# Performance work log

Measured on AMD Instinct MI355X. Metric: run time of the kernel, lower is better.

The kernel has to match this reference:

```python
import jax, jax.numpy as jnp
import numpy as np

N_INPUTS, N_NEURONS, N_OUTPUTS = 64, 128, 32
T = 1048576


def setup_inputs() -> dict:
    key = jax.random.key(0)
    ks = jax.random.split(key, 7)
    s = 1.0 / np.sqrt(N_NEURONS)  # PyTorch RNNCell init: U(-1/sqrt(hidden), 1/sqrt(hidden))
    x = jax.random.normal(ks[0], (T, N_INPUTS), dtype=jnp.float32)
    W_ih = jax.random.uniform(ks[1], (N_NEURONS, N_INPUTS), jnp.float32, -s, s)
    W_hh = jax.random.uniform(ks[2], (N_NEURONS, N_NEURONS), jnp.float32, -s, s)
    b_ih = jax.random.uniform(ks[3], (N_NEURONS,), jnp.float32, -s, s)
    b_hh = jax.random.uniform(ks[4], (N_NEURONS,), jnp.float32, -s, s)
    W_out = jax.random.uniform(ks[5], (N_NEURONS, N_OUTPUTS), jnp.float32, -0.01, 0.01)
    b_out = jax.random.uniform(ks[6], (N_OUTPUTS,), jnp.float32, -0.01, 0.01)
    h0 = jnp.zeros((N_NEURONS,), dtype=jnp.float32)  # self.hidden_state, never updated
    return {"external_input_tensor": x, "W_ih": W_ih, "W_hh": W_hh,
            "b_ih": b_ih, "b_hh": b_hh, "W_out": W_out, "b_out": b_out, "h0": h0}


def reference(external_input_tensor, W_ih, W_hh, b_ih, b_hh, W_out, b_out, h0):
    # Original torch loop never updates self.hidden_state, so every step uses h0:
    # h_t = relu(x_t @ W_ih^T + b_ih + h0 @ W_hh^T + b_hh); out_t = h_t @ W_out + b_out
    # This is fully parallel over T, so vectorize the whole thing.
    hidden_drive = h0 @ W_hh.T + b_ih + b_hh  # [N_NEURONS]
    h = jax.nn.relu(external_input_tensor @ W_ih.T + hidden_drive)  # [T, N_NEURONS]
    return h @ W_out + b_out  # [T, N_OUTPUTS]
```

## Files before the change

kernel.cpp:

```cpp
#include <hip/hip_runtime.h>
#include <hip/hip_bf16.h>


typedef __attribute__((ext_vector_type(8))) short short8v;
typedef __attribute__((ext_vector_type(4))) short short4v;
typedef __attribute__((ext_vector_type(4))) float f32x4;

static __device__ __forceinline__ short f2bs(float f) {
    union { __hip_bfloat16 b; short s; } u;
    u.b = __float2bfloat16(f);
    return u.s;
}

static __device__ __forceinline__ short8v pack8(f32x4 a, f32x4 b) {
    short8v r;
    r[0] = f2bs(a[0]); r[1] = f2bs(a[1]); r[2] = f2bs(a[2]); r[3] = f2bs(a[3]);
    r[4] = f2bs(b[0]); r[5] = f2bs(b[1]); r[6] = f2bs(b[2]); r[7] = f2bs(b[3]);
    return r;
}

__global__ void hd_kernel(const float* __restrict__ Whh, const float* __restrict__ bih,
                          const float* __restrict__ bhh, const float* __restrict__ h0,
                          float* __restrict__ hd) {
    int n = threadIdx.x;
    if (n < 128) {
        float s = bih[n] + bhh[n];
        for (int k = 0; k < 128; ++k) s += Whh[n * 128 + k] * h0[k];
        hd[n] = s;
    }
}

#define HSTRIDE 136

__global__ __launch_bounds__(256, 2)
void rnn_fused(const float* __restrict__ x, const float* __restrict__ Wih,
               const float* __restrict__ Wout, const float* __restrict__ bout,
               const float* __restrict__ hd, float* __restrict__ out, int T) {
    const int lane = threadIdx.x & 63;
    const int wave = threadIdx.x >> 6;
    const int c    = lane & 15;
    const int q    = lane >> 4;
    const int nwaves = gridDim.x * 4;
    const int gw     = blockIdx.x * 4 + wave;
    const int NT     = T >> 4;

    __shared__ __align__(16) short hbuf[4 * 16 * HSTRIDE];
    short* hrow = &hbuf[wave * (16 * HSTRIDE)];

    short8v a_w[8][2];
#pragma unroll
    for (int mt = 0; mt < 8; ++mt) {
#pragma unroll
        for (int kc = 0; kc < 2; ++kc) {
            const float* p = Wih + (mt * 16 + c) * 64 + kc * 32 + q * 8;
            f32x4 f0 = *(const f32x4*)p;
            f32x4 f1 = *(const f32x4*)(p + 4);
            a_w[mt][kc] = pack8(f0, f1);
        }
    }

    short8v a_o[2][4];
#pragma unroll
    for (int mt = 0; mt < 2; ++mt) {
#pragma unroll
        for (int kc = 0; kc < 4; ++kc) {
            short8v v;
#pragma unroll
            for (int j = 0; j < 8; ++j)
                v[j] = f2bs(Wout[(kc * 32 + q * 8 + j) * 32 + mt * 16 + c]);
            a_o[mt][kc] = v;
        }
    }

    f32x4 hd4[8];
#pragma unroll
    for (int mt = 0; mt < 8; ++mt) hd4[mt] = *(const f32x4*)(hd + mt * 16 + q * 4);
    f32x4 bo4[2];
#pragma unroll
    for (int mt = 0; mt < 2; ++mt) bo4[mt] = *(const f32x4*)(bout + mt * 16 + q * 4);

    f32x4 xa, xb, xc2, xd;
    int tile = gw;
    if (tile < NT) {
        const f32x4* xp = (const f32x4*)(x + ((size_t)(tile * 16 + c)) * 64 + q * 8);
        xa = xp[0]; xb = xp[1]; xc2 = xp[8]; xd = xp[9];
    }

    while (tile < NT) {
        f32x4 c0 = xa, c1 = xb, c2 = xc2, c3 = xd;
        const int nxt = tile + nwaves;
        if (nxt < NT) {
            const f32x4* xp = (const f32x4*)(x + ((size_t)(nxt * 16 + c)) * 64 + q * 8);
            xa = xp[0]; xb = xp[1]; xc2 = xp[8]; xd = xp[9];
        }

        short8v xb0 = pack8(c0, c1);
        short8v xb1 = pack8(c2, c3);

        f32x4 acc[8];
#pragma unroll
        for (int mt = 0; mt < 8; ++mt) {
            acc[mt] = __builtin_amdgcn_mfma_f32_16x16x32_bf16(a_w[mt][0], xb0, hd4[mt], 0, 0, 0);
            acc[mt] = __builtin_amdgcn_mfma_f32_16x16x32_bf16(a_w[mt][1], xb1, acc[mt], 0, 0, 0);
        }

#pragma unroll
        for (int mt = 0; mt < 8; ++mt) {
            short4v s;
            s[0] = f2bs(fmaxf(acc[mt][0], 0.f));
            s[1] = f2bs(fmaxf(acc[mt][1], 0.f));
            s[2] = f2bs(fmaxf(acc[mt][2], 0.f));
            s[3] = f2bs(fmaxf(acc[mt][3], 0.f));
            *(short4v*)&hrow[c * HSTRIDE + mt * 16 + q * 4] = s;
        }

        short8v hb0 = *(const short8v*)&hrow[c * HSTRIDE + 0 * 32 + q * 8];
        short8v hb1 = *(const short8v*)&hrow[c * HSTRIDE + 1 * 32 + q * 8];
        short8v hb2 = *(const short8v*)&hrow[c * HSTRIDE + 2 * 32 + q * 8];
        short8v hb3 = *(const short8v*)&hrow[c * HSTRIDE + 3 * 32 + q * 8];

        f32x4 o0 = bo4[0], o1 = bo4[1];
        o0 = __builtin_amdgcn_mfma_f32_16x16x32_bf16(a_o[0][0], hb0, o0, 0, 0, 0);
        o1 = __builtin_amdgcn_mfma_f32_16x16x32_bf16(a_o[1][0], hb0, o1, 0, 0, 0);
        o0 = __builtin_amdgcn_mfma_f32_16x16x32_bf16(a_o[0][1], hb1, o0, 0, 0, 0);
        o1 = __builtin_amdgcn_mfma_f32_16x16x32_bf16(a_o[1][1], hb1, o1, 0, 0, 0);
        o0 = __builtin_amdgcn_mfma_f32_16x16x32_bf16(a_o[0][2], hb2, o0, 0, 0, 0);
        o1 = __builtin_amdgcn_mfma_f32_16x16x32_bf16(a_o[1][2], hb2, o1, 0, 0, 0);
        o0 = __builtin_amdgcn_mfma_f32_16x16x32_bf16(a_o[0][3], hb3, o0, 0, 0, 0);
        o1 = __builtin_amdgcn_mfma_f32_16x16x32_bf16(a_o[1][3], hb3, o1, 0, 0, 0);

        float* op = out + ((size_t)(tile * 16 + c)) * 32 + q * 4;
        *(f32x4*)(op)      = o0;
        *(f32x4*)(op + 16) = o1;

        tile = nxt;
    }
}

extern "C" void kernel_launch(void* const* d_in, const int* in_sizes, int n_in,
                              void* d_out, int out_size, void* d_ws, size_t ws_size,
                              hipStream_t stream) {
    const float* x    = (const float*)d_in[0];
    const float* Wih  = (const float*)d_in[1];
    const float* Whh  = (const float*)d_in[2];
    const float* bih  = (const float*)d_in[3];
    const float* bhh  = (const float*)d_in[4];
    const float* Wout = (const float*)d_in[5];
    const float* bout = (const float*)d_in[6];
    const float* h0   = (const float*)d_in[7];
    float* out = (float*)d_out;
    float* hd  = (float*)d_ws;

    const int T = in_sizes[0] / 64;

    hd_kernel<<<1, 128, 0, stream>>>(Whh, bih, bhh, h0, hd);
    rnn_fused<<<512, 256, 0, stream>>>(x, Wih, Wout, bout, hd, out, T);
}
```

Baseline: 410.8 us.

## Fuse hidden-drive into main kernel, deepen x prefetch, use cheaper bf16 packing

Removes the separate single-block hd_kernel launch: each block computes the hidden drive into shared memory before the main loop. The x prefetch becomes two tiles deep with alternating register sets, and loads and stores use nontemporal hints. The bf16 conversion is replaced by a manual round-half-up bit pack of two floats, which is cheaper but not round-to-nearest-even and does not handle NaN. Every block now redundantly computes the 128x128 matvec, adding a small prologue cost in exchange for dropping one launch.

```diff
diff --git a/kernel.cpp b/kernel.cpp
--- a/kernel.cpp
+++ b/kernel.cpp
@@ -6,38 +6,40 @@
 typedef __attribute__((ext_vector_type(4))) short short4v;
 typedef __attribute__((ext_vector_type(4))) float f32x4;
 
-static __device__ __forceinline__ short f2bs(float f) {
-    union { __hip_bfloat16 b; short s; } u;
-    u.b = __float2bfloat16(f);
-    return u.s;
+static __device__ __forceinline__ unsigned pk_bf16(float lo, float hi) {
+    unsigned ul = __float_as_uint(lo), uh = __float_as_uint(hi);
+    return ((ul + 0x8000u) >> 16) | ((uh + 0x8000u) & 0xffff0000u);
 }
 
-static __device__ __forceinline__ short8v pack8(f32x4 a, f32x4 b) {
-    short8v r;
-    r[0] = f2bs(a[0]); r[1] = f2bs(a[1]); r[2] = f2bs(a[2]); r[3] = f2bs(a[3]);
-    r[4] = f2bs(b[0]); r[5] = f2bs(b[1]); r[6] = f2bs(b[2]); r[7] = f2bs(b[3]);
-    return r;
+static __device__ __forceinline__ short8v pack8v(f32x4 a, f32x4 b) {
+    union { unsigned u[4]; short8v s; } r;
+    r.u[0] = pk_bf16(a[0], a[1]);
+    r.u[1] = pk_bf16(a[2], a[3]);
+    r.u[2] = pk_bf16(b[0], b[1]);
+    r.u[3] = pk_bf16(b[2], b[3]);
+    return r.s;
 }
 
-__global__ void hd_kernel(const float* __restrict__ Whh, const float* __restrict__ bih,
-                          const float* __restrict__ bhh, const float* __restrict__ h0,
-                          float* __restrict__ hd) {
-    int n = threadIdx.x;
-    if (n < 128) {
-        float s = bih[n] + bhh[n];
-        for (int k = 0; k < 128; ++k) s += Whh[n * 128 + k] * h0[k];
-        hd[n] = s;
-    }
+static __device__ __forceinline__ short4v relu_pack4(f32x4 v) {
+    union { unsigned u[2]; short4v s; } r;
+    r.u[0] = pk_bf16(fmaxf(v[0], 0.f), fmaxf(v[1], 0.f));
+    r.u[1] = pk_bf16(fmaxf(v[2], 0.f), fmaxf(v[3], 0.f));
+    return r.s;
 }
+
+#define NTL(p) __builtin_nontemporal_load((const f32x4*)(p))
 
 #define HSTRIDE 136
 
 __global__ __launch_bounds__(256, 2)
 void rnn_fused(const float* __restrict__ x, const float* __restrict__ Wih,
-               const float* __restrict__ Wout, const float* __restrict__ bout,
-               const float* __restrict__ hd, float* __restrict__ out, int T) {
-    const int lane = threadIdx.x & 63;
-    const int wave = threadIdx.x >> 6;
+               const float* __restrict__ Whh, const float* __restrict__ bih,
+               const float* __restrict__ bhh, const float* __restrict__ Wout,
+               const float* __restrict__ bout, const float* __restrict__ h0,
+               float* __restrict__ out, int T) {
+    const int tid  = threadIdx.x;
+    const int lane = tid & 63;
+    const int wave = tid >> 6;
     const int c    = lane & 15;
     const int q    = lane >> 4;
     const int nwaves = gridDim.x * 4;
@@ -45,6 +47,7 @@
     const int NT     = T >> 4;
 
     __shared__ __align__(16) short hbuf[4 * 16 * HSTRIDE];
+    __shared__ __align__(16) float hdLDS[128];
     short* hrow = &hbuf[wave * (16 * HSTRIDE)];
 
     short8v a_w[8][2];
@@ -53,9 +56,7 @@
 #pragma unroll
         for (int kc = 0; kc < 2; ++kc) {
             const float* p = Wih + (mt * 16 + c) * 64 + kc * 32 + q * 8;
-            f32x4 f0 = *(const f32x4*)p;
-            f32x4 f1 = *(const f32x4*)(p + 4);
-            a_w[mt][kc] = pack8(f0, f1);
+            a_w[mt][kc] = pack8v(*(const f32x4*)p, *(const f32x4*)(p + 4));
         }
     }
 
@@ -64,55 +65,48 @@
     for (int mt = 0; mt < 2; ++mt) {
 #pragma unroll
         for (int kc = 0; kc < 4; ++kc) {
-            short8v v;
+            union { unsigned u[4]; short8v s; } v;
 #pragma unroll
-            for (int j = 0; j < 8; ++j)
-                v[j] = f2bs(Wout[(kc * 32 + q * 8 + j) * 32 + mt * 16 + c]);
-            a_o[mt][kc] = v;
+            for (int j = 0; j < 4; ++j) {
+                float f0 = Wout[(kc * 32 + q * 8 + 2 * j) * 32 + mt * 16 + c];
+                float f1 = Wout[(kc * 32 + q * 8 + 2 * j + 1) * 32 + mt * 16 + c];
+                v.u[j] = pk_bf16(f0, f1);
+            }
+            a_o[mt][kc] = v.s;
         }
     }
 
-    f32x4 hd4[8];
-#pragma unroll
-    for (int mt = 0; mt < 8; ++mt) hd4[mt] = *(const f32x4*)(hd + mt * 16 + q * 4);
     f32x4 bo4[2];
 #pragma unroll
     for (int mt = 0; mt < 2; ++mt) bo4[mt] = *(const f32x4*)(bout + mt * 16 + q * 4);
 
-    f32x4 xa, xb, xc2, xd;
-    int tile = gw;
-    if (tile < NT) {
-        const f32x4* xp = (const f32x4*)(x + ((size_t)(tile * 16 + c)) * 64 + q * 8);
-        xa = xp[0]; xb = xp[1]; xc2 = xp[8]; xd = xp[9];
+    if (tid < 128) {
+        float s = bih[tid] + bhh[tid];
+        const f32x4* wr = (const f32x4*)(Whh + tid * 128);
+        const f32x4* hr = (const f32x4*)h0;
+#pragma unroll 8
+        for (int k = 0; k < 32; ++k) {
+            f32x4 w = wr[k], h = hr[k];
+            s += w[0] * h[0] + w[1] * h[1] + w[2] * h[2] + w[3] * h[3];
+        }
+        hdLDS[tid] = s;
     }
+    __syncthreads();
 
-    while (tile < NT) {
-        f32x4 c0 = xa, c1 = xb, c2 = xc2, c3 = xd;
-        const int nxt = tile + nwaves;
-        if (nxt < NT) {
-            const f32x4* xp = (const f32x4*)(x + ((size_t)(nxt * 16 + c)) * 64 + q * 8);
-            xa = xp[0]; xb = xp[1]; xc2 = xp[8]; xd = xp[9];
-        }
+    f32x4 hd4[8];
+#pragma unroll
+    for (int mt = 0; mt < 8; ++mt) hd4[mt] = *(const f32x4*)&hdLDS[mt * 16 + q * 4];
 
-        short8v xb0 = pack8(c0, c1);
-        short8v xb1 = pack8(c2, c3);
-
+    auto body = [&](short8v xb0, short8v xb1, size_t row) {
         f32x4 acc[8];
 #pragma unroll
         for (int mt = 0; mt < 8; ++mt) {
             acc[mt] = __builtin_amdgcn_mfma_f32_16x16x32_bf16(a_w[mt][0], xb0, hd4[mt], 0, 0, 0);
             acc[mt] = __builtin_amdgcn_mfma_f32_16x16x32_bf16(a_w[mt][1], xb1, acc[mt], 0, 0, 0);
         }
-
 #pragma unroll
-        for (int mt = 0; mt < 8; ++mt) {
-            short4v s;
-            s[0] = f2bs(fmaxf(acc[mt][0], 0.f));
-            s[1] = f2bs(fmaxf(acc[mt][1], 0.f));
-            s[2] = f2bs(fmaxf(acc[mt][2], 0.f));
-            s[3] = f2bs(fmaxf(acc[mt][3], 0.f));
-            *(short4v*)&hrow[c * HSTRIDE + mt * 16 + q * 4] = s;
-        }
+        for (int mt = 0; mt < 8; ++mt)
+            *(short4v*)&hrow[c * HSTRIDE + mt * 16 + q * 4] = relu_pack4(acc[mt]);
 
         short8v hb0 = *(const short8v*)&hrow[c * HSTRIDE + 0 * 32 + q * 8];
         short8v hb1 = *(const short8v*)&hrow[c * HSTRIDE + 1 * 32 + q * 8];
@@ -129,11 +123,42 @@
         o0 = __builtin_amdgcn_mfma_f32_16x16x32_bf16(a_o[0][3], hb3, o0, 0, 0, 0);
         o1 = __builtin_amdgcn_mfma_f32_16x16x32_bf16(a_o[1][3], hb3, o1, 0, 0, 0);
 
-        float* op = out + ((size_t)(tile * 16 + c)) * 32 + q * 4;
-        *(f32x4*)(op)      = o0;
-        *(f32x4*)(op + 16) = o1;
+        float* op = out + row * 32 + q * 4;
+        __builtin_nontemporal_store(o0, (f32x4*)op);
+        __builtin_nontemporal_store(o1, (f32x4*)(op + 16));
+    };
 
-        tile = nxt;
+    int niter = (gw < NT) ? (NT - gw + nwaves - 1) / nwaves : 0;
+    const size_t rowstep = (size_t)nwaves * 16 * 64;
+    const size_t tstep   = (size_t)nwaves * 16;
+    size_t row = (size_t)gw * 16 + c;
+    const float* xcur = x + row * 64 + q * 8;
+
+    f32x4 A0, A1, A2, A3, B0, B1, B2, B3;
+    if (niter > 0) { A0 = NTL(xcur); A1 = NTL(xcur + 4); A2 = NTL(xcur + 32); A3 = NTL(xcur + 36); }
+    if (niter > 1) {
+        const float* p = xcur + rowstep;
+        B0 = NTL(p); B1 = NTL(p + 4); B2 = NTL(p + 32); B3 = NTL(p + 36);
+    }
+
+    int it = 0;
+    while (it < niter) {
+        short8v xb0 = pack8v(A0, A1), xb1 = pack8v(A2, A3);
+        if (it + 2 < niter) {
+            const float* p = xcur + 2 * rowstep;
+            A0 = NTL(p); A1 = NTL(p + 4); A2 = NTL(p + 32); A3 = NTL(p + 36);
+        }
+        body(xb0, xb1, row);
+        ++it; row += tstep; xcur += rowstep;
+        if (it >= niter) break;
+
+        xb0 = pack8v(B0, B1); xb1 = pack8v(B2, B3);
+        if (it + 2 < niter) {
+            const float* p = xcur + 2 * rowstep;
+            B0 = NTL(p); B1 = NTL(p + 4); B2 = NTL(p + 32); B3 = NTL(p + 36);
+        }
+        body(xb0, xb1, row);
+        ++it; row += tstep; xcur += rowstep;
     }
 }
 
@@ -149,10 +174,8 @@
     const float* bout = (const float*)d_in[6];
     const float* h0   = (const float*)d_in[7];
     float* out = (float*)d_out;
-    float* hd  = (float*)d_ws;
 
     const int T = in_sizes[0] / 64;
 
-    hd_kernel<<<1, 128, 0, stream>>>(Whh, bih, bhh, h0, hd);
-    rnn_fused<<<512, 256, 0, stream>>>(x, Wih, Wout, bout, hd, out, T);
+    rnn_fused<<<512, 256, 0, stream>>>(x, Wih, Whh, bih, bhh, Wout, bout, h0, out, T);
 }
```

Result: slower. 420.9 us (+2.5%).
